# Kernel optimization log

Measured on AMD Instinct MI355X. Metric: run time of the kernel, lower is better.

The kernel has to match this reference:

```python
import jax, jax.numpy as jnp
import numpy as np

B, LP, LQ, H = 16, 2048, 2048, 1024

def setup_inputs() -> dict:
    key = jax.random.key(0)
    k1, k2, k3 = jax.random.split(key, 3)
    proj_p = jax.random.normal(k1, (B, LP, H), dtype=jnp.float32)
    proj_q = jax.random.normal(k2, (B, LQ, H), dtype=jnp.float32)
    # nn.Linear(hidden_size, hidden_size): W stored as [out, in], y = x @ W.T + b
    W = jax.random.normal(k3, (H, H), dtype=jnp.float32) * (1.0 / np.sqrt(H))
    b = jnp.zeros((H,), dtype=jnp.float32)
    return {"proj_p": proj_p, "proj_q": proj_q, "W": W, "b": b}

def reference(proj_p, proj_q, W, b):
    # trans_q = Linear(proj_q)
    trans_q = jnp.einsum('bqh,oh->bqo', proj_q, W) + b            # [B,LQ,H]
    # UNscaled attention scores: proj_p @ trans_q^T
    att_weights = jnp.einsum('bph,bqh->bpq', proj_p, trans_q)     # [B,LP,LQ]
    att_norm = jax.nn.softmax(att_weights, axis=-1)
    att_vec = jnp.einsum('bpq,bqh->bph', att_norm, proj_q)        # [B,LP,H]
    # same linear weight reused, then ReLU
    out = jax.nn.relu(jnp.einsum('bph,oh->bpo', att_vec, W) + b)
    return out
```

## Files before the change

### kernel.cpp

```cpp
#include <hip/hip_runtime.h>

typedef _Float16 f16;
typedef _Float16 f16x8 __attribute__((ext_vector_type(8)));
typedef _Float16 f16x4 __attribute__((ext_vector_type(4)));
typedef float    f32x16 __attribute__((ext_vector_type(16)));

#define GLDS(gp, lp) __builtin_amdgcn_global_load_lds( \
    (const __attribute__((address_space(1))) void*)(gp), \
    (__attribute__((address_space(3))) void*)(lp), 16, 0, 0)

template<typename OUT_T, bool BIAS, bool RELU>
__global__ __launch_bounds__(512, 2)
void gemm_bt2(const f16* __restrict__ A, const f16* __restrict__ Bm,
              OUT_T* __restrict__ C, const float* __restrict__ bias,
              int M, int N, int K, long sA, long sB, long sC)
{
    constexpr int TSZ = 256 * 64;
    __shared__ alignas(16) f16 As[2 * TSZ];
    __shared__ alignas(16) f16 Bs[2 * TSZ];

    int bx = blockIdx.x, by = blockIdx.y;
    {
        const int gx = gridDim.x;
        const int l = by * gx + bx;
        const int W = gx * 8;
        const int ygrp = l / W;
        const int rem = l - ygrp * W;
        bx = rem >> 3;
        by = ygrp * 8 + (rem & 7);
    }
    const int z = blockIdx.z;
    A  += (long)z * sA;
    Bm += (long)z * sB;
    C  += (long)z * sC;

    const int tid  = threadIdx.x;
    const int wid  = tid >> 6;
    const int lane = tid & 63;
    const int lr = lane & 31;
    const int lh = lane >> 5;
    const int m0 = by * 256;
    const int n0 = bx * 256;
    const int wm = (wid >> 2) * 128;
    const int wn = (wid & 3) * 64;

    const int sr = tid >> 3;
    const int sg = ((tid & 7) ^ (sr & 7)) * 8;
    const f16* agS = A  + (long)(m0 + sr) * K + sg;
    const f16* bgS = Bm + (long)(n0 + sr) * K + sg;
    f16* aD = As + wid * (8 * 64);
    f16* bD = Bs + wid * (8 * 64);

    const int s7  = lr & 7;
    const int xs0 = ((0 + lh) ^ s7) * 8;
    const int xs1 = ((2 + lh) ^ s7) * 8;
    const int xs2 = ((4 + lh) ^ s7) * 8;
    const int xs3 = ((6 + lh) ^ s7) * 8;
    const f16* aR = As + (wm + lr) * 64;
    const f16* bR = Bs + (wn + lr) * 64;

    f32x16 acc[4][2];
#pragma unroll
    for (int mi = 0; mi < 4; ++mi)
#pragma unroll
        for (int ni = 0; ni < 2; ++ni)
#pragma unroll
            for (int r = 0; r < 16; ++r) acc[mi][ni][r] = 0.f;

    f16x8 b00, b01, b02, b03, b10, b11, b12, b13;

    const int NT = K >> 6;

#define GAc(buf, R0, kt) GLDS(agS + (long)(R0) * K + (kt), aD + (buf) * TSZ + (R0) * 64)
#define GBc(buf, R0, kt) GLDS(bgS + (long)(R0) * K + (kt), bD + (buf) * TSZ + (R0) * 64)

    GBc(0,   0, 0);  GBc(0,  64, 0);  GBc(0, 128, 0);  GBc(0, 192, 0);
    GAc(0,   0, 0);  GAc(0,  64, 0);  GAc(0, 128, 0);  GAc(0, 192, 0);
    GBc(1,   0, 64); GBc(1,  64, 64); GBc(1, 128, 64); GBc(1, 192, 64);
    GAc(1,   0, 64); GAc(1, 128, 64);
    asm volatile("s_waitcnt vmcnt(6)" ::: "memory");
    __builtin_amdgcn_s_barrier();

#define MFMA8(mi) \
    acc[mi][0] = __builtin_amdgcn_mfma_f32_32x32x16_f16(af0, b00, acc[mi][0], 0, 0, 0); \
    acc[mi][1] = __builtin_amdgcn_mfma_f32_32x32x16_f16(af0, b10, acc[mi][1], 0, 0, 0); \
    acc[mi][0] = __builtin_amdgcn_mfma_f32_32x32x16_f16(af1, b01, acc[mi][0], 0, 0, 0); \
    acc[mi][1] = __builtin_amdgcn_mfma_f32_32x32x16_f16(af1, b11, acc[mi][1], 0, 0, 0); \
    acc[mi][0] = __builtin_amdgcn_mfma_f32_32x32x16_f16(af2, b02, acc[mi][0], 0, 0, 0); \
    acc[mi][1] = __builtin_amdgcn_mfma_f32_32x32x16_f16(af2, b12, acc[mi][1], 0, 0, 0); \
    acc[mi][0] = __builtin_amdgcn_mfma_f32_32x32x16_f16(af3, b03, acc[mi][0], 0, 0, 0); \
    acc[mi][1] = __builtin_amdgcn_mfma_f32_32x32x16_f16(af3, b13, acc[mi][1], 0, 0, 0);

#define PH(buf, mi, VW, ...) { \
    f16x8 af0 = *(const f16x8*)(aR + (buf) * TSZ + (mi) * 2048 + xs0); \
    f16x8 af1 = *(const f16x8*)(aR + (buf) * TSZ + (mi) * 2048 + xs1); \
    f16x8 af2 = *(const f16x8*)(aR + (buf) * TSZ + (mi) * 2048 + xs2); \
    f16x8 af3 = *(const f16x8*)(aR + (buf) * TSZ + (mi) * 2048 + xs3); \
    if ((mi) == 0) { \
        b00 = *(const f16x8*)(bR + (buf) * TSZ + xs0); \
        b01 = *(const f16x8*)(bR + (buf) * TSZ + xs1); \
        b02 = *(const f16x8*)(bR + (buf) * TSZ + xs2); \
        b03 = *(const f16x8*)(bR + (buf) * TSZ + xs3); \
        b10 = *(const f16x8*)(bR + (buf) * TSZ + 2048 + xs0); \
        b11 = *(const f16x8*)(bR + (buf) * TSZ + 2048 + xs1); \
        b12 = *(const f16x8*)(bR + (buf) * TSZ + 2048 + xs2); \
        b13 = *(const f16x8*)(bR + (buf) * TSZ + 2048 + xs3); \
    } \
    __VA_ARGS__ \
    __builtin_amdgcn_s_barrier(); \
    __builtin_amdgcn_s_setprio(1); \
    MFMA8(mi) \
    __builtin_amdgcn_s_setprio(0); \
    if (VW) { asm volatile("s_waitcnt vmcnt(6)" ::: "memory"); } \
    __builtin_amdgcn_s_barrier(); \
}

    for (int i = 0; i < NT / 2; ++i) {
        const long k1 = (long)(2 * i + 1) << 6;
        const long kA = (2 * i + 2 < NT) ? ((long)(2 * i + 2) << 6) : 0;
        const long kB = (2 * i + 3 < NT) ? ((long)(2 * i + 3) << 6) : 0;
        PH(0, 0, 0, GAc(1,  64, k1); GAc(1, 192, k1);)
        PH(0, 1, 0, GBc(0,   0, kA); GBc(0,  64, kA);)
        PH(0, 2, 0, GBc(0, 128, kA); GBc(0, 192, kA);)
        PH(0, 3, 1, GAc(0,   0, kA); GAc(0, 128, kA);)
        PH(1, 0, 0, GAc(0,  64, kA); GAc(0, 192, kA);)
        PH(1, 1, 0, GBc(1,   0, kB); GBc(1,  64, kB);)
        PH(1, 2, 0, GBc(1, 128, kB); GBc(1, 192, kB);)
        PH(1, 3, 1, GAc(1,   0, kB); GAc(1, 128, kB);)
    }

    asm volatile("s_waitcnt vmcnt(0)" ::: "memory");

#pragma unroll
    for (int ni = 0; ni < 2; ++ni) {
        const int gc = n0 + wn + ni * 32 + lr;
        const float bv = BIAS ? bias[gc] : 0.0f;
#pragma unroll
        for (int mi = 0; mi < 4; ++mi) {
#pragma unroll
            for (int r = 0; r < 16; ++r) {
                const int row = (r & 3) + 8 * (r >> 2) + 4 * lh;
                const int gr = m0 + wm + mi * 32 + row;
                float v = acc[mi][ni][r] + bv;
                if (RELU) v = fmaxf(v, 0.0f);
                C[(long)gr * N + gc] = (OUT_T)v;
            }
        }
    }
#undef PH
#undef MFMA8
#undef GAc
#undef GBc
}

template<typename OUT_T, bool BIAS, bool RELU>
__global__ __launch_bounds__(512, 2)
void gemm_bt3(const f16* __restrict__ A, const f16* __restrict__ Bm,
              OUT_T* __restrict__ C, const float* __restrict__ bias,
              int M, int N, int K, long sA, long sB, long sC)
{
    constexpr int TSA = 256 * 64;
    constexpr int TSB = 128 * 64;
    __shared__ alignas(16) f16 As[2 * TSA];
    __shared__ alignas(16) f16 Bs[2 * TSB];

    int bx = blockIdx.x, by = blockIdx.y;
    {
        const int gx = gridDim.x;
        const int l = by * gx + bx;
        const int W = gx * 8;
        const int ygrp = l / W;
        const int rem = l - ygrp * W;
        bx = rem >> 3;
        by = ygrp * 8 + (rem & 7);
    }
    const int z = blockIdx.z;
    A  += (long)z * sA;
    Bm += (long)z * sB;
    C  += (long)z * sC;

    const int tid  = threadIdx.x;
    const int wid  = tid >> 6;
    const int lane = tid & 63;
    const int lr = lane & 31;
    const int lh = lane >> 5;
    const int m0 = by * 256;
    const int n0 = bx * 128;
    const int wm = (wid >> 1) * 64;
    const int wn = (wid & 1) * 64;

    const int sr = tid >> 3;
    const int sg = ((tid & 7) ^ (sr & 7)) * 8;
    const f16* agS = A  + (long)(m0 + sr) * K + sg;
    const f16* bgS = Bm + (long)(n0 + sr) * K + sg;
    f16* aD = As + wid * (8 * 64);
    f16* bD = Bs + wid * (8 * 64);

    const int s7  = lr & 7;
    const int xs0 = ((0 + lh) ^ s7) * 8;
    const int xs1 = ((2 + lh) ^ s7) * 8;
    const int xs2 = ((4 + lh) ^ s7) * 8;
    const int xs3 = ((6 + lh) ^ s7) * 8;
    const f16* aR = As + (wm + lr) * 64;
    const f16* bR = Bs + (wn + lr) * 64;

    f32x16 acc[2][2];
#pragma unroll
    for (int mi = 0; mi < 2; ++mi)
#pragma unroll
        for (int ni = 0; ni < 2; ++ni)
#pragma unroll
            for (int r = 0; r < 16; ++r) acc[mi][ni][r] = 0.f;

    f16x8 b00, b01, b02, b03, b10, b11, b12, b13;

    const int NT = K >> 6;

#define GA3(buf, R0, kt) GLDS(agS + (long)(R0) * K + (kt), aD + (buf) * TSA + (R0) * 64)
#define GB3(buf, R0, kt) GLDS(bgS + (long)(R0) * K + (kt), bD + (buf) * TSB + (R0) * 64)

    GB3(0,   0, 0);  GB3(0,  64, 0);
    GA3(0,   0, 0);  GA3(0,  64, 0);  GA3(0, 128, 0);  GA3(0, 192, 0);
    GB3(1,   0, 64); GB3(1,  64, 64);
    asm volatile("s_waitcnt vmcnt(2)" ::: "memory");
    __builtin_amdgcn_s_barrier();

#define MFMA8_3(mi) \
    acc[mi][0] = __builtin_amdgcn_mfma_f32_32x32x16_f16(af0, b00, acc[mi][0], 0, 0, 0); \
    acc[mi][1] = __builtin_amdgcn_mfma_f32_32x32x16_f16(af0, b10, acc[mi][1], 0, 0, 0); \
    acc[mi][0] = __builtin_amdgcn_mfma_f32_32x32x16_f16(af1, b01, acc[mi][0], 0, 0, 0); \
    acc[mi][1] = __builtin_amdgcn_mfma_f32_32x32x16_f16(af1, b11, acc[mi][1], 0, 0, 0); \
    acc[mi][0] = __builtin_amdgcn_mfma_f32_32x32x16_f16(af2, b02, acc[mi][0], 0, 0, 0); \
    acc[mi][1] = __builtin_amdgcn_mfma_f32_32x32x16_f16(af2, b12, acc[mi][1], 0, 0, 0); \
    acc[mi][0] = __builtin_amdgcn_mfma_f32_32x32x16_f16(af3, b03, acc[mi][0], 0, 0, 0); \
    acc[mi][1] = __builtin_amdgcn_mfma_f32_32x32x16_f16(af3, b13, acc[mi][1], 0, 0, 0);

#define PH3(buf, mi, VW, ...) { \
    f16x8 af0 = *(const f16x8*)(aR + (buf) * TSA + (mi) * 2048 + xs0); \
    f16x8 af1 = *(const f16x8*)(aR + (buf) * TSA + (mi) * 2048 + xs1); \
    f16x8 af2 = *(const f16x8*)(aR + (buf) * TSA + (mi) * 2048 + xs2); \
    f16x8 af3 = *(const f16x8*)(aR + (buf) * TSA + (mi) * 2048 + xs3); \
    if ((mi) == 0) { \
        b00 = *(const f16x8*)(bR + (buf) * TSB + xs0); \
        b01 = *(const f16x8*)(bR + (buf) * TSB + xs1); \
        b02 = *(const f16x8*)(bR + (buf) * TSB + xs2); \
        b03 = *(const f16x8*)(bR + (buf) * TSB + xs3); \
        b10 = *(const f16x8*)(bR + (buf) * TSB + 2048 + xs0); \
        b11 = *(const f16x8*)(bR + (buf) * TSB + 2048 + xs1); \
        b12 = *(const f16x8*)(bR + (buf) * TSB + 2048 + xs2); \
        b13 = *(const f16x8*)(bR + (buf) * TSB + 2048 + xs3); \
    } \
    __VA_ARGS__ \
    __builtin_amdgcn_s_barrier(); \
    __builtin_amdgcn_s_setprio(1); \
    MFMA8_3(mi) \
    __builtin_amdgcn_s_setprio(0); \
    if (VW) { asm volatile("s_waitcnt vmcnt(2)" ::: "memory"); } \
    __builtin_amdgcn_s_barrier(); \
}

    for (int i = 0; i < NT / 2; ++i) {
        const long k1 = (long)(2 * i + 1) << 6;
        const long kA = (2 * i + 2 < NT) ? ((long)(2 * i + 2) << 6) : 0;
        const long kB = (2 * i + 3 < NT) ? ((long)(2 * i + 3) << 6) : 0;
        PH3(0, 0, 0, GA3(1,   0, k1); GA3(1,  64, k1); GA3(1, 128, k1); GA3(1, 192, k1);)
        PH3(0, 1, 1, GB3(0,   0, kA); GB3(0,  64, kA);)
        PH3(1, 0, 0, GA3(0,   0, kA); GA3(0,  64, kA); GA3(0, 128, kA); GA3(0, 192, kA);)
        PH3(1, 1, 1, GB3(1,   0, kB); GB3(1,  64, kB);)
    }

    asm volatile("s_waitcnt vmcnt(0)" ::: "memory");

#pragma unroll
    for (int ni = 0; ni < 2; ++ni) {
        const int gc = n0 + wn + ni * 32 + lr;
        const float bv = BIAS ? bias[gc] : 0.0f;
#pragma unroll
        for (int mi = 0; mi < 2; ++mi) {
#pragma unroll
            for (int r = 0; r < 16; ++r) {
                const int row = (r & 3) + 8 * (r >> 2) + 4 * lh;
                const int gr = m0 + wm + mi * 32 + row;
                float v = acc[mi][ni][r] + bv;
                if (RELU) v = fmaxf(v, 0.0f);
                C[(long)gr * N + gc] = (OUT_T)v;
            }
        }
    }
#undef PH3
#undef MFMA8_3
#undef GA3
#undef GB3
}

__global__ __launch_bounds__(256)
void cast_f32_f16(const float* __restrict__ X, f16* __restrict__ Y)
{
    const long i = ((long)blockIdx.x * 256 + threadIdx.x) * 8;
    float4 a = *(const float4*)(X + i);
    float4 b = *(const float4*)(X + i + 4);
    f16x8 h = {(f16)a.x, (f16)a.y, (f16)a.z, (f16)a.w,
               (f16)b.x, (f16)b.y, (f16)b.z, (f16)b.w};
    *(f16x8*)(Y + i) = h;
}

__global__ __launch_bounds__(256)
void cast_q_dual(const float* __restrict__ X, f16* __restrict__ Yrow,
                 f16* __restrict__ Ytr)
{
    __shared__ f16 t[64][72];
    const float* Xb = X + (long)blockIdx.z * (2048L * 1024);
    f16* Yrb = Yrow + (long)blockIdx.z * (2048L * 1024);
    f16* Ytb = Ytr  + (long)blockIdx.z * (1024L * 2048);
    const int r0 = blockIdx.y * 64;
    const int c0 = blockIdx.x * 64;
    const int tid = threadIdx.x;
    const int tr = tid >> 4;
    const int tc = (tid & 15) * 4;
#pragma unroll
    for (int rr = 0; rr < 64; rr += 16) {
        float4 v = *(const float4*)(Xb + (long)(r0 + tr + rr) * 1024 + c0 + tc);
        f16x4 h = {(f16)v.x, (f16)v.y, (f16)v.z, (f16)v.w};
        *(f16x4*)&t[tr + rr][tc] = h;
        *(f16x4*)(Yrb + (long)(r0 + tr + rr) * 1024 + c0 + tc) = h;
    }
    __syncthreads();
#pragma unroll
    for (int rr = 0; rr < 64; rr += 16) {
        const int orow = tr + rr;
        f16x4 o = {t[tc + 0][orow], t[tc + 1][orow], t[tc + 2][orow], t[tc + 3][orow]};
        *(f16x4*)(Ytb + (long)(c0 + orow) * 2048 + r0 + tc) = o;
    }
}

__global__ __launch_bounds__(256)
void softmax_p(const float* __restrict__ S, f16* __restrict__ P)
{
    const long row = blockIdx.x;
    const float* s = S + row * 2048;
    f16* p = P + row * 2048;
    const int tid = threadIdx.x;
    const int wid = tid >> 6, lane = tid & 63;

    float4 a = *(const float4*)(s + tid * 8);
    float4 b = *(const float4*)(s + tid * 8 + 4);
    float v[8] = {a.x, a.y, a.z, a.w, b.x, b.y, b.z, b.w};

    float m = v[0];
#pragma unroll
    for (int j = 1; j < 8; ++j) m = fmaxf(m, v[j]);
#pragma unroll
    for (int off = 32; off > 0; off >>= 1) m = fmaxf(m, __shfl_xor(m, off, 64));

    __shared__ float red[8];
    if (lane == 0) red[wid] = m;
    __syncthreads();
    m = fmaxf(fmaxf(red[0], red[1]), fmaxf(red[2], red[3]));

    float sum = 0.f;
#pragma unroll
    for (int j = 0; j < 8; ++j) { v[j] = __expf(v[j] - m); sum += v[j]; }
#pragma unroll
    for (int off = 32; off > 0; off >>= 1) sum += __shfl_xor(sum, off, 64);
    if (lane == 0) red[4 + wid] = sum;
    __syncthreads();
    sum = red[4] + red[5] + red[6] + red[7];

    const float inv = 1.0f / sum;
    f16x8 h = {(f16)(v[0] * inv), (f16)(v[1] * inv), (f16)(v[2] * inv), (f16)(v[3] * inv),
               (f16)(v[4] * inv), (f16)(v[5] * inv), (f16)(v[6] * inv), (f16)(v[7] * inv)};
    *(f16x8*)(p + tid * 8) = h;
}

extern "C" void kernel_launch(void* const* d_in, const int* in_sizes, int n_in,
                              void* d_out, int out_size, void* d_ws, size_t ws_size,
                              hipStream_t stream)
{
    const float* proj_p = (const float*)d_in[0];
    const float* proj_q = (const float*)d_in[1];
    const float* W      = (const float*)d_in[2];
    const float* bias   = (const float*)d_in[3];
    float* out = (float*)d_out;

    constexpr long Bc = 16, L = 2048, H = 1024, NB = 4;
    constexpr long nPQ = Bc * L * H;

    char* ws = (char*)d_ws;
    f16*   pB  = (f16*)(ws + 0L);
    f16*   qB  = (f16*)(ws + 67108864L);
    f16*   qBt = (f16*)(ws + 134217728L);
    f16*   tQ  = (f16*)(ws + 201326592L);
    f16*   aV  = (f16*)(ws + 268435456L);
    f16*   Wb  = (f16*)(ws + 335544320L);
    float* S   = (float*)(ws + 337641472L);
    f16*   P   = (f16*)(ws + 404750336L);

    cast_f32_f16<<<nPQ / (256 * 8), 256, 0, stream>>>(proj_p, pB);
    cast_f32_f16<<<(H * H) / (256 * 8), 256, 0, stream>>>(W, Wb);
    cast_q_dual<<<dim3(16, 32, 16), 256, 0, stream>>>(proj_q, qB, qBt);

    gemm_bt2<f16, true, false><<<dim3(H / 256, (Bc * L) / 256, 1), 512, 0, stream>>>(
        qB, Wb, tQ, bias, (int)(Bc * L), (int)H, (int)H, 0, 0, 0);

    for (int c = 0; c < 4; ++c) {
        const long boff = (long)c * NB * L * H;
        gemm_bt2<float, false, false><<<dim3(L / 256, L / 256, NB), 512, 0, stream>>>(
            pB + boff, tQ + boff, S, nullptr, (int)L, (int)L, (int)H,
            L * H, L * H, L * L);
        softmax_p<<<NB * L, 256, 0, stream>>>(S, P);
        gemm_bt3<f16, false, false><<<dim3(H / 128, L / 256, NB), 512, 0, stream>>>(
            P, qBt + (long)c * NB * H * L, aV + boff, nullptr, (int)L, (int)H, (int)L,
            L * L, H * L, L * H);
    }

    gemm_bt2<float, false, true><<<dim3(H / 256, (Bc * L) / 256, 1), 512, 0, stream>>>(
        aV, Wb, out, bias, (int)(Bc * L), (int)H, (int)H, 0, 0, 0);
}
```

Baseline: 941.0 us.

## Use 4 waves with 128x128 warp tiles in gemm_bt2

gemm_bt2 now runs with 256 threads (4 waves) instead of 512, and each wave computes a 128x128 sub-tile instead of 128x64. The accumulators grow to 4x4 32x32 tiles per wave, and the B fragments are read once per k-tile. The global-to-LDS load schedule is redone as 32-row chunks because there are fewer threads per load, and the vmcnt waits are adjusted to match. This raises register reuse per MFMA and halves the LDS B reads, at the cost of much higher register pressure (256 accumulator VGPRs), one block per CU, and less latency hiding.

```diff
diff --git a/kernel.cpp b/kernel.cpp
--- a/kernel.cpp
+++ b/kernel.cpp
@@ -10,7 +10,7 @@
     (__attribute__((address_space(3))) void*)(lp), 16, 0, 0)
 
 template<typename OUT_T, bool BIAS, bool RELU>
-__global__ __launch_bounds__(512, 2)
+__global__ __launch_bounds__(256, 1)
 void gemm_bt2(const f16* __restrict__ A, const f16* __restrict__ Bm,
               OUT_T* __restrict__ C, const float* __restrict__ bias,
               int M, int N, int K, long sA, long sB, long sC)
@@ -41,8 +41,8 @@
     const int lh = lane >> 5;
     const int m0 = by * 256;
     const int n0 = bx * 256;
-    const int wm = (wid >> 2) * 128;
-    const int wn = (wid & 3) * 64;
+    const int wm = (wid >> 1) * 128;
+    const int wn = (wid & 1) * 128;
 
     const int sr = tid >> 3;
     const int sg = ((tid & 7) ^ (sr & 7)) * 8;
@@ -59,59 +59,79 @@
     const f16* aR = As + (wm + lr) * 64;
     const f16* bR = Bs + (wn + lr) * 64;
 
-    f32x16 acc[4][2];
+    f32x16 acc[4][4];
 #pragma unroll
     for (int mi = 0; mi < 4; ++mi)
 #pragma unroll
-        for (int ni = 0; ni < 2; ++ni)
+        for (int ni = 0; ni < 4; ++ni)
 #pragma unroll
             for (int r = 0; r < 16; ++r) acc[mi][ni][r] = 0.f;
 
     f16x8 b00, b01, b02, b03, b10, b11, b12, b13;
+    f16x8 b20, b21, b22, b23, b30, b31, b32, b33;
 
     const int NT = K >> 6;
 
-#define GAc(buf, R0, kt) GLDS(agS + (long)(R0) * K + (kt), aD + (buf) * TSZ + (R0) * 64)
-#define GBc(buf, R0, kt) GLDS(bgS + (long)(R0) * K + (kt), bD + (buf) * TSZ + (R0) * 64)
-
-    GBc(0,   0, 0);  GBc(0,  64, 0);  GBc(0, 128, 0);  GBc(0, 192, 0);
-    GAc(0,   0, 0);  GAc(0,  64, 0);  GAc(0, 128, 0);  GAc(0, 192, 0);
-    GBc(1,   0, 64); GBc(1,  64, 64); GBc(1, 128, 64); GBc(1, 192, 64);
-    GAc(1,   0, 64); GAc(1, 128, 64);
-    asm volatile("s_waitcnt vmcnt(6)" ::: "memory");
+#define GA2(buf, R0, kt) GLDS(agS + (long)(R0) * K + (kt), aD + (buf) * TSZ + (R0) * 64)
+#define GB2(buf, R0, kt) GLDS(bgS + (long)(R0) * K + (kt), bD + (buf) * TSZ + (R0) * 64)
+#define AHEAD(buf, kt) GA2(buf,   0, kt); GA2(buf,  32, kt); GA2(buf, 128, kt); GA2(buf, 160, kt);
+#define ATAIL(buf, kt) GA2(buf,  64, kt); GA2(buf,  96, kt); GA2(buf, 192, kt); GA2(buf, 224, kt);
+#define BHA(buf, kt)   GB2(buf,   0, kt); GB2(buf,  32, kt); GB2(buf,  64, kt); GB2(buf,  96, kt);
+#define BHB(buf, kt)   GB2(buf, 128, kt); GB2(buf, 160, kt); GB2(buf, 192, kt); GB2(buf, 224, kt);
+
+    BHA(0, 0)  BHB(0, 0)  AHEAD(0, 0)  ATAIL(0, 0)
+    BHA(1, 64) BHB(1, 64) AHEAD(1, 64)
+    asm volatile("s_waitcnt vmcnt(12)" ::: "memory");
     __builtin_amdgcn_s_barrier();
 
-#define MFMA8(mi) \
+#define BFREAD(buf) \
+    b00 = *(const f16x8*)(bR + (buf) * TSZ +    0 + xs0); \
+    b01 = *(const f16x8*)(bR + (buf) * TSZ +    0 + xs1); \
+    b02 = *(const f16x8*)(bR + (buf) * TSZ +    0 + xs2); \
+    b03 = *(const f16x8*)(bR + (buf) * TSZ +    0 + xs3); \
+    b10 = *(const f16x8*)(bR + (buf) * TSZ + 2048 + xs0); \
+    b11 = *(const f16x8*)(bR + (buf) * TSZ + 2048 + xs1); \
+    b12 = *(const f16x8*)(bR + (buf) * TSZ + 2048 + xs2); \
+    b13 = *(const f16x8*)(bR + (buf) * TSZ + 2048 + xs3); \
+    b20 = *(const f16x8*)(bR + (buf) * TSZ + 4096 + xs0); \
+    b21 = *(const f16x8*)(bR + (buf) * TSZ + 4096 + xs1); \
+    b22 = *(const f16x8*)(bR + (buf) * TSZ + 4096 + xs2); \
+    b23 = *(const f16x8*)(bR + (buf) * TSZ + 4096 + xs3); \
+    b30 = *(const f16x8*)(bR + (buf) * TSZ + 6144 + xs0); \
+    b31 = *(const f16x8*)(bR + (buf) * TSZ + 6144 + xs1); \
+    b32 = *(const f16x8*)(bR + (buf) * TSZ + 6144 + xs2); \
+    b33 = *(const f16x8*)(bR + (buf) * TSZ + 6144 + xs3);
+
+#define MFMA16(mi) \
     acc[mi][0] = __builtin_amdgcn_mfma_f32_32x32x16_f16(af0, b00, acc[mi][0], 0, 0, 0); \
     acc[mi][1] = __builtin_amdgcn_mfma_f32_32x32x16_f16(af0, b10, acc[mi][1], 0, 0, 0); \
+    acc[mi][2] = __builtin_amdgcn_mfma_f32_32x32x16_f16(af0, b20, acc[mi][2], 0, 0, 0); \
+    acc[mi][3] = __builtin_amdgcn_mfma_f32_32x32x16_f16(af0, b30, acc[mi][3], 0, 0, 0); \
     acc[mi][0] = __builtin_amdgcn_mfma_f32_32x32x16_f16(af1, b01, acc[mi][0], 0, 0, 0); \
     acc[mi][1] = __builtin_amdgcn_mfma_f32_32x32x16_f16(af1, b11, acc[mi][1], 0, 0, 0); \
+    acc[mi][2] = __builtin_amdgcn_mfma_f32_32x32x16_f16(af1, b21, acc[mi][2], 0, 0, 0); \
+    acc[mi][3] = __builtin_amdgcn_mfma_f32_32x32x16_f16(af1, b31, acc[mi][3], 0, 0, 0); \
     acc[mi][0] = __builtin_amdgcn_mfma_f32_32x32x16_f16(af2, b02, acc[mi][0], 0, 0, 0); \
     acc[mi][1] = __builtin_amdgcn_mfma_f32_32x32x16_f16(af2, b12, acc[mi][1], 0, 0, 0); \
+    acc[mi][2] = __builtin_amdgcn_mfma_f32_32x32x16_f16(af2, b22, acc[mi][2], 0, 0, 0); \
+    acc[mi][3] = __builtin_amdgcn_mfma_f32_32x32x16_f16(af2, b32, acc[mi][3], 0, 0, 0); \
     acc[mi][0] = __builtin_amdgcn_mfma_f32_32x32x16_f16(af3, b03, acc[mi][0], 0, 0, 0); \
-    acc[mi][1] = __builtin_amdgcn_mfma_f32_32x32x16_f16(af3, b13, acc[mi][1], 0, 0, 0);
-
-#define PH(buf, mi, VW, ...) { \
+    acc[mi][1] = __builtin_amdgcn_mfma_f32_32x32x16_f16(af3, b13, acc[mi][1], 0, 0, 0); \
+    acc[mi][2] = __builtin_amdgcn_mfma_f32_32x32x16_f16(af3, b23, acc[mi][2], 0, 0, 0); \
+    acc[mi][3] = __builtin_amdgcn_mfma_f32_32x32x16_f16(af3, b33, acc[mi][3], 0, 0, 0);
+
+#define PH(buf, mi, RB, VW, ...) { \
     f16x8 af0 = *(const f16x8*)(aR + (buf) * TSZ + (mi) * 2048 + xs0); \
     f16x8 af1 = *(const f16x8*)(aR + (buf) * TSZ + (mi) * 2048 + xs1); \
     f16x8 af2 = *(const f16x8*)(aR + (buf) * TSZ + (mi) * 2048 + xs2); \
     f16x8 af3 = *(const f16x8*)(aR + (buf) * TSZ + (mi) * 2048 + xs3); \
-    if ((mi) == 0) { \
-        b00 = *(const f16x8*)(bR + (buf) * TSZ + xs0); \
-        b01 = *(const f16x8*)(bR + (buf) * TSZ + xs1); \
-        b02 = *(const f16x8*)(bR + (buf) * TSZ + xs2); \
-        b03 = *(const f16x8*)(bR + (buf) * TSZ + xs3); \
-        b10 = *(const f16x8*)(bR + (buf) * TSZ + 2048 + xs0); \
-        b11 = *(const f16x8*)(bR + (buf) * TSZ + 2048 + xs1); \
-        b12 = *(const f16x8*)(bR + (buf) * TSZ + 2048 + xs2); \
-        b13 = *(const f16x8*)(bR + (buf) * TSZ + 2048 + xs3); \
-    } \
+    if (RB) { BFREAD(buf) } \
     __VA_ARGS__ \
     __builtin_amdgcn_s_barrier(); \
     __builtin_amdgcn_s_setprio(1); \
-    MFMA8(mi) \
+    MFMA16(mi) \
     __builtin_amdgcn_s_setprio(0); \
-    if (VW) { asm volatile("s_waitcnt vmcnt(6)" ::: "memory"); } \
+    if (VW) { asm volatile("s_waitcnt vmcnt(12)" ::: "memory"); } \
     __builtin_amdgcn_s_barrier(); \
 }
 
@@ -119,20 +139,20 @@
         const long k1 = (long)(2 * i + 1) << 6;
         const long kA = (2 * i + 2 < NT) ? ((long)(2 * i + 2) << 6) : 0;
         const long kB = (2 * i + 3 < NT) ? ((long)(2 * i + 3) << 6) : 0;
-        PH(0, 0, 0, GAc(1,  64, k1); GAc(1, 192, k1);)
-        PH(0, 1, 0, GBc(0,   0, kA); GBc(0,  64, kA);)
-        PH(0, 2, 0, GBc(0, 128, kA); GBc(0, 192, kA);)
-        PH(0, 3, 1, GAc(0,   0, kA); GAc(0, 128, kA);)
-        PH(1, 0, 0, GAc(0,  64, kA); GAc(0, 192, kA);)
-        PH(1, 1, 0, GBc(1,   0, kB); GBc(1,  64, kB);)
-        PH(1, 2, 0, GBc(1, 128, kB); GBc(1, 192, kB);)
-        PH(1, 3, 1, GAc(1,   0, kB); GAc(1, 128, kB);)
+        PH(0, 0, 1, 0, ATAIL(1, k1))
+        PH(0, 1, 0, 0, BHA(0, kA))
+        PH(0, 2, 0, 0, BHB(0, kA))
+        PH(0, 3, 0, 1, AHEAD(0, kA))
+        PH(1, 0, 1, 0, ATAIL(0, kA))
+        PH(1, 1, 0, 0, BHA(1, kB))
+        PH(1, 2, 0, 0, BHB(1, kB))
+        PH(1, 3, 0, 1, AHEAD(1, kB))
     }
 
     asm volatile("s_waitcnt vmcnt(0)" ::: "memory");
 
 #pragma unroll
-    for (int ni = 0; ni < 2; ++ni) {
+    for (int ni = 0; ni < 4; ++ni) {
         const int gc = n0 + wn + ni * 32 + lr;
         const float bv = BIAS ? bias[gc] : 0.0f;
 #pragma unroll
@@ -148,9 +168,14 @@
         }
     }
 #undef PH
-#undef MFMA8
-#undef GAc
-#undef GBc
+#undef MFMA16
+#undef BFREAD
+#undef AHEAD
+#undef ATAIL
+#undef BHA
+#undef BHB
+#undef GA2
+#undef GB2
 }
 
 template<typename OUT_T, bool BIAS, bool RELU>
@@ -399,12 +424,12 @@
     cast_f32_f16<<<(H * H) / (256 * 8), 256, 0, stream>>>(W, Wb);
     cast_q_dual<<<dim3(16, 32, 16), 256, 0, stream>>>(proj_q, qB, qBt);
 
-    gemm_bt2<f16, true, false><<<dim3(H / 256, (Bc * L) / 256, 1), 512, 0, stream>>>(
+    gemm_bt2<f16, true, false><<<dim3(H / 256, (Bc * L) / 256, 1), 256, 0, stream>>>(
         qB, Wb, tQ, bias, (int)(Bc * L), (int)H, (int)H, 0, 0, 0);
 
     for (int c = 0; c < 4; ++c) {
         const long boff = (long)c * NB * L * H;
-        gemm_bt2<float, false, false><<<dim3(L / 256, L / 256, NB), 512, 0, stream>>>(
+        gemm_bt2<float, false, false><<<dim3(L / 256, L / 256, NB), 256, 0, stream>>>(
             pB + boff, tQ + boff, S, nullptr, (int)L, (int)L, (int)H,
             L * H, L * H, L * L);
         softmax_p<<<NB * L, 256, 0, stream>>>(S, P);
@@ -413,6 +438,6 @@
             L * L, H * L, L * H);
     }
 
-    gemm_bt2<float, false, true><<<dim3(H / 256, (Bc * L) / 256, 1), 512, 0, stream>>>(
+    gemm_bt2<float, false, true><<<dim3(H / 256, (Bc * L) / 256, 1), 256, 0, stream>>>(
         aV, Wb, out, bias, (int)(Bc * L), (int)H, (int)H, 0, 0, 0);
 }
```

Result: slower. 964.5 us (+2.5%).
